# Kernel tuning notes

Hardware: AMD Instinct MI355X
Metric: run time of the kernel (lower is better)

Reference implementation:

```python
import jax, jax.numpy as jnp
import numpy as np

B_SZ = 4; SEQ = 2048; SPLIT = 1024
D_MODEL = 512; N_LAYERS = 2; EXPAND = 2
D_INNER = EXPAND * D_MODEL          # 1024
HEADDIM = 64; NHEADS = D_INNER // HEADDIM   # 16
DSTATE = 64; CONV = 4; CHUNK = 256
D_INPROJ = 2 * D_INNER + 2 * DSTATE + NHEADS   # z, xBC, dt
CONVDIM = D_INNER + 2 * DSTATE
NHID = 1024; NOUT = 10; CA_HEADS = 4; CA_HD = D_MODEL // CA_HEADS


def _ln(x, w, b, eps=1e-5):
    m = jnp.mean(x, -1, keepdims=True)
    v = jnp.mean(jnp.square(x - m), -1, keepdims=True)
    return (x - m) * jax.lax.rsqrt(v + eps) * w + b


def _segsum(x):
    # x: (..., T) -> (..., T, T) lower-triangular cumulative segment sums
    T = x.shape[-1]
    xc = jnp.cumsum(x, -1)
    ss = xc[..., :, None] - xc[..., None, :]
    mask = jnp.tril(jnp.ones((T, T), bool))
    return jnp.where(mask, ss, -jnp.inf)


def _ssd(x, A, B, C):
    # chunked SSD (Mamba2). x:(b,l,h,p) dt-prescaled; A:(b,l,h)=dt*A; B,C:(b,l,n)
    b, l, h, p = x.shape
    n = B.shape[-1]
    c = l // CHUNK
    x = x.reshape(b, c, CHUNK, h, p)
    A = jnp.transpose(A.reshape(b, c, CHUNK, h), (0, 1, 3, 2))   # (b,c,h,L)
    B = B.reshape(b, c, CHUNK, n)
    C = C.reshape(b, c, CHUNK, n)
    A_cum = jnp.cumsum(A, -1)
    Lmat = jnp.exp(_segsum(A))                                    # (b,c,h,L,L)
    Y_diag = jnp.einsum('bcln,bcsn,bchls,bcshp->bclhp', C, B, Lmat, x)
    decay_states = jnp.exp(A_cum[..., -1:] - A_cum)               # (b,c,h,L)
    states = jnp.einsum('bcln,bchl,bclhp->bchpn', B, decay_states, x)
    chunk_decay = jnp.exp(A_cum[..., -1])                         # (b,c,h)
    def step(hprev, inp):
        dec, s = inp
        return hprev * dec[..., None, None] + s, hprev
    init = jnp.zeros((b, h, p, n), x.dtype)
    _, prev = jax.lax.scan(step, init,
                           (jnp.moveaxis(chunk_decay, 1, 0), jnp.moveaxis(states, 1, 0)))
    prev = jnp.moveaxis(prev, 0, 1)                               # (b,c,h,p,n) state at chunk start
    Y_off = jnp.einsum('bcln,bchpn,bchl->bclhp', C, prev, jnp.exp(A_cum))
    return (Y_diag + Y_off).reshape(b, l, h, p)


def _mamba2_dir(u, Win, cw, cb, dtb, Alog, Dp, gw, Wout):
    b, l, _ = u.shape
    zxbcdt = u @ Win
    z, xBC, dt_raw = jnp.split(zxbcdt, [D_INNER, D_INNER + CONVDIM], -1)
    # causal depthwise conv, kernel CONV
    xp = jnp.pad(xBC, ((0, 0), (CONV - 1, 0), (0, 0)))
    xc = cb + sum(xp[:, k:k + l, :] * cw[:, k] for k in range(CONV))
    xc = jax.nn.silu(xc)
    x, Bm, Cm = jnp.split(xc, [D_INNER, D_INNER + DSTATE], -1)
    dt = jax.nn.softplus(dt_raw + dtb)                            # (b,l,h)
    A = -jnp.exp(Alog)                                            # (h,)
    xh = x.reshape(b, l, NHEADS, HEADDIM)
    y = _ssd(xh * dt[..., None], dt * A, Bm, Cm) + Dp[None, None, :, None] * xh
    y = y.reshape(b, l, D_INNER) * jax.nn.silu(z)                 # gated
    y = y * jax.lax.rsqrt(jnp.mean(jnp.square(y), -1, keepdims=True) + 1e-5) * gw
    return y @ Wout


def _cross_attn(q_in, c_in, nqw, nqb, nkvw, nkvb, qw, qb, kw, kb, vw, vb, ow, ob):
    res = q_in
    q = _ln(q_in, nqw, nqb)
    c = _ln(c_in, nkvw, nkvb)
    Bq, Nq, D = q.shape
    Nc = c.shape[1]
    Q = (q @ qw + qb).reshape(Bq, Nq, CA_HEADS, CA_HD)
    K = (c @ kw + kb).reshape(Bq, Nc, CA_HEADS, CA_HD)
    V = (c @ vw + vb).reshape(Bq, Nc, CA_HEADS, CA_HD)
    attn = jax.nn.softmax(jnp.einsum('bqhd,bkhd->bhqk', Q, K) / np.float32(np.sqrt(CA_HD)), -1)
    out = jnp.einsum('bhqk,bkhd->bqhd', attn, V).reshape(Bq, Nq, D)
    return res + out @ ow + ob


def _forward(x_enc, split_pos, in_proj_w, conv_w, conv_b, dt_bias, A_log, D_param,
             gnorm_w, out_proj_w, norm_w, norm_b, normf_w, normf_b,
             ca_nq_w, ca_nq_b, ca_nkv_w, ca_nkv_b, ca_qw, ca_qb, ca_kw, ca_kb,
             ca_vw, ca_vb, ca_ow, ca_ob, qp_w, qp_b, cp_w, cp_b,
             dec1_w, dec1_b, dec2_w, dec2_b):
    h = x_enc
    res = None
    for i in range(N_LAYERS):
        res = h if res is None else h + res
        hn = _ln(res, norm_w[i], norm_b[i])
        fwd = _mamba2_dir(hn, in_proj_w[i, 0], conv_w[i, 0], conv_b[i, 0], dt_bias[i, 0],
                          A_log[i, 0], D_param[i, 0], gnorm_w[i, 0], out_proj_w[i, 0])
        bwd = _mamba2_dir(jnp.flip(hn, 1), in_proj_w[i, 1], conv_w[i, 1], conv_b[i, 1],
                          dt_bias[i, 1], A_log[i, 1], D_param[i, 1], gnorm_w[i, 1], out_proj_w[i, 1])
        h = fwd + jnp.flip(bwd, 1)
    res = h + res
    h = _ln(res, normf_w, normf_b)
    context = h[:, :split_pos]
    query = h[:, split_pos:]
    q = query @ qp_w + qp_b
    c = context @ cp_w + cp_b
    out = _cross_attn(q, c, ca_nq_w, ca_nq_b, ca_nkv_w, ca_nkv_b,
                      ca_qw, ca_qb, ca_kw, ca_kb, ca_vw, ca_vb, ca_ow, ca_ob)
    out = jax.nn.gelu(out @ dec1_w + dec1_b, approximate=False) @ dec2_w + dec2_b
    return out


def setup_inputs() -> dict:
    key = jax.random.key(0)
    ks = iter(jax.random.split(key, 64))
    def nrm(shape, scale=0.02):
        return jax.random.normal(next(ks), shape, jnp.float32) * scale
    L2 = (N_LAYERS, 2)
    inp = {}
    inp['x_enc'] = jax.random.normal(next(ks), (B_SZ, SEQ, D_MODEL), jnp.float32)
    inp['split_pos'] = SPLIT
    inp['in_proj_w'] = nrm(L2 + (D_MODEL, D_INPROJ))
    inp['conv_w'] = nrm(L2 + (CONVDIM, CONV), 0.1)
    inp['conv_b'] = jnp.zeros(L2 + (CONVDIM,), jnp.float32)
    inp['dt_bias'] = nrm(L2 + (NHEADS,), 0.5)
    inp['A_log'] = jnp.log(jnp.broadcast_to(jnp.arange(1, NHEADS + 1, dtype=jnp.float32), L2 + (NHEADS,)))
    inp['D_param'] = jnp.ones(L2 + (NHEADS,), jnp.float32)
    inp['gnorm_w'] = jnp.ones(L2 + (D_INNER,), jnp.float32)
    inp['out_proj_w'] = nrm(L2 + (D_INNER, D_MODEL))
    inp['norm_w'] = jnp.ones((N_LAYERS, D_MODEL), jnp.float32)
    inp['norm_b'] = jnp.zeros((N_LAYERS, D_MODEL), jnp.float32)
    inp['normf_w'] = jnp.ones((D_MODEL,), jnp.float32)
    inp['normf_b'] = jnp.zeros((D_MODEL,), jnp.float32)
    inp['ca_nq_w'] = jnp.ones((D_MODEL,), jnp.float32); inp['ca_nq_b'] = jnp.zeros((D_MODEL,), jnp.float32)
    inp['ca_nkv_w'] = jnp.ones((D_MODEL,), jnp.float32); inp['ca_nkv_b'] = jnp.zeros((D_MODEL,), jnp.float32)
    for nm in ['ca_qw', 'ca_kw', 'ca_vw', 'ca_ow']:
        inp[nm] = nrm((D_MODEL, D_MODEL))
    for nm in ['ca_qb', 'ca_kb', 'ca_vb', 'ca_ob']:
        inp[nm] = jnp.zeros((D_MODEL,), jnp.float32)
    inp['qp_w'] = nrm((D_MODEL, D_MODEL)); inp['qp_b'] = jnp.zeros((D_MODEL,), jnp.float32)
    inp['cp_w'] = nrm((D_MODEL, D_MODEL)); inp['cp_b'] = jnp.zeros((D_MODEL,), jnp.float32)
    inp['dec1_w'] = nrm((D_MODEL, NHID)); inp['dec1_b'] = jnp.zeros((NHID,), jnp.float32)
    inp['dec2_w'] = nrm((NHID, NOUT)); inp['dec2_b'] = jnp.zeros((NOUT,), jnp.float32)
    return inp


def reference(x_enc, split_pos, in_proj_w, conv_w, conv_b, dt_bias, A_log, D_param,
              gnorm_w, out_proj_w, norm_w, norm_b, normf_w, normf_b,
              ca_nq_w, ca_nq_b, ca_nkv_w, ca_nkv_b, ca_qw, ca_qb, ca_kw, ca_kb,
              ca_vw, ca_vb, ca_ow, ca_ob, qp_w, qp_b, cp_w, cp_b,
              dec1_w, dec1_b, dec2_w, dec2_b):
    return _forward(x_enc, split_pos, in_proj_w, conv_w, conv_b, dt_bias, A_log, D_param,
                    gnorm_w, out_proj_w, norm_w, norm_b, normf_w, normf_b,
                    ca_nq_w, ca_nq_b, ca_nkv_w, ca_nkv_b, ca_qw, ca_qb, ca_kw, ca_kb,
                    ca_vw, ca_vb, ca_ow, ca_ob, qp_w, qp_b, cp_w, cp_b,
                    dec1_w, dec1_b, dec2_w, dec2_b)
```

## Files before the change

kernel.cpp:

```cpp
#include <hip/hip_runtime.h>
#include <hip/hip_bf16.h>

#define BS 4
#define SEQL 2048
#define DM 512
#define DIN 1024
#define NH 16
#define HD 64
#define DST 64
#define NC 8
#define CKS 256
#define DIP 2192
#define CVD 1152
#define NROWS (BS*SEQL)
#define NTOK (BS*SEQL*DM)

typedef unsigned short u16;
typedef __bf16 bf16x8 __attribute__((ext_vector_type(8)));
typedef float f32x4 __attribute__((ext_vector_type(4)));

__device__ __forceinline__ u16 cvt_bf16(float f){
  unsigned int x = __float_as_uint(f);
  unsigned int r = x + 0x7fffu + ((x>>16)&1u);
  return (u16)(r>>16);
}
__device__ __forceinline__ float bf2f(u16 u){
  return __uint_as_float(((unsigned int)u)<<16);
}

__global__ void k_add_flip(float* __restrict__ dst, const float* __restrict__ src, int flip){
  int i = blockIdx.x*256 + threadIdx.x;
  if(i >= NTOK) return;
  int d = i & (DM-1);
  int l = (i >> 9) & (SEQL-1);
  int b = i >> 20;
  int sl = flip ? (SEQL-1-l) : l;
  dst[i] += src[(b*SEQL + sl)*DM + d];
}

__global__ void k_flip(float* __restrict__ dst, const float* __restrict__ src){
  int i = blockIdx.x*256 + threadIdx.x;
  if(i >= NTOK) return;
  int d = i & (DM-1);
  int l = (i >> 9) & (SEQL-1);
  int b = i >> 20;
  dst[i] = src[(b*SEQL + (SEQL-1-l))*DM + d];
}

__global__ void k_cvt(const float* __restrict__ src, u16* __restrict__ dst, int n4){
  int i = blockIdx.x*256 + threadIdx.x;
  if(i >= n4) return;
  float4 f = reinterpret_cast<const float4*>(src)[i];
  ushort4 o; o.x=cvt_bf16(f.x); o.y=cvt_bf16(f.y); o.z=cvt_bf16(f.z); o.w=cvt_bf16(f.w);
  reinterpret_cast<ushort4*>(dst)[i] = o;
}

__global__ void k_ln(const float* __restrict__ X, const float* __restrict__ w,
                     const float* __restrict__ bb, float* __restrict__ O){
  int row = blockIdx.x, tid = threadIdx.x;
  const float* x = X + (size_t)row*DM;
  float* o = O + (size_t)row*DM;
  float s=0.f, s2=0.f;
  for(int j=tid;j<DM;j+=256){ float v=x[j]; s+=v; s2+=v*v; }
  __shared__ float r1[256], r2[256];
  r1[tid]=s; r2[tid]=s2; __syncthreads();
  for(int off=128;off>0;off>>=1){
    if(tid<off){ r1[tid]+=r1[tid+off]; r2[tid]+=r2[tid+off]; }
    __syncthreads();
  }
  float m = r1[0]*(1.f/DM);
  float var = r2[0]*(1.f/DM) - m*m;
  float inv = rsqrtf(var + 1e-5f);
  for(int j=tid;j<DM;j+=256) o[j] = (x[j]-m)*inv*w[j] + bb[j];
}

__global__ void k_rms(float* __restrict__ Y, const float* __restrict__ gw){
  int row = blockIdx.x, tid = threadIdx.x;
  float* y = Y + (size_t)row*DIN;
  float ss=0.f;
  for(int j=tid;j<DIN;j+=256){ float v=y[j]; ss+=v*v; }
  __shared__ float red[256];
  red[tid]=ss; __syncthreads();
  for(int off=128;off>0;off>>=1){
    if(tid<off) red[tid]+=red[tid+off];
    __syncthreads();
  }
  float inv = rsqrtf(red[0]*(1.f/DIN) + 1e-5f);
  for(int j=tid;j<DIN;j+=256) y[j] = y[j]*inv*gw[j];
}

__global__ void k_dec2(const float* __restrict__ D1, const float* __restrict__ w,
                       const float* __restrict__ bb, float* __restrict__ out){
  int row = blockIdx.x, tid = threadIdx.x;
  int lane = tid & 63, wave = tid >> 6;
  const float* x = D1 + (size_t)row*1024;
  float acc[10];
  #pragma unroll
  for(int o=0;o<10;o++) acc[o]=0.f;
  for(int j=tid;j<1024;j+=256){
    float v = x[j];
    const float* wr = w + (size_t)j*10;
    #pragma unroll
    for(int o=0;o<10;o++) acc[o] += v*wr[o];
  }
  __shared__ float red[4][10];
  #pragma unroll
  for(int o=0;o<10;o++){
    float v = acc[o];
    #pragma unroll
    for(int s=32;s>0;s>>=1) v += __shfl_down(v, s, 64);
    if(lane==0) red[wave][o] = v;
  }
  __syncthreads();
  if(tid < 10)
    out[(size_t)row*10 + tid] = red[0][tid]+red[1][tid]+red[2][tid]+red[3][tid] + bb[tid];
}

__global__ void k_wt2(const float* __restrict__ src, u16* __restrict__ dst,
                      int K, int N, int lds){
  __shared__ float t[32][33];
  int n0 = blockIdx.x*32, k0 = blockIdx.y*32;
  int tx = threadIdx.x, ty = threadIdx.y;
  #pragma unroll
  for(int i=0;i<32;i+=8){
    int k = k0+ty+i, n = n0+tx;
    t[ty+i][tx] = (n<N) ? src[(size_t)k*lds+n] : 0.f;
  }
  __syncthreads();
  #pragma unroll
  for(int i=0;i<32;i+=8){
    int n = n0+ty+i, k = k0+tx;
    if(n<N) dst[(size_t)n*K+k] = cvt_bf16(t[tx][ty+i]);
  }
}

__global__ void k_vtb(const float* __restrict__ VV, u16* __restrict__ VT){
  __shared__ float t[32][33];
  int z = blockIdx.z, b = z>>2, h = z&3;
  const float* src = VV + (size_t)b*524288 + h*128;
  u16* dst = VT + (size_t)z*131072;
  int n0 = blockIdx.x*32, k0 = blockIdx.y*32;
  int tx = threadIdx.x, ty = threadIdx.y;
  #pragma unroll
  for(int i=0;i<32;i+=8){
    int k = k0+ty+i, n = n0+tx;
    t[ty+i][tx] = src[(size_t)k*512+n];
  }
  __syncthreads();
  #pragma unroll
  for(int i=0;i<32;i+=8){
    int n = n0+ty+i, k = k0+tx;
    dst[(size_t)n*1024+k] = cvt_bf16(t[tx][ty+i]);
  }
}

__global__ void k_xdtt(const float* __restrict__ XC, const float* __restrict__ DT,
                       u16* __restrict__ XdT){
  __shared__ float t[32][33];
  int z = blockIdx.z;
  int h = z & 15, bc = z >> 4;
  int b = bc >> 3, c = bc & 7;
  int p0 = blockIdx.x*32, s0 = blockIdx.y*32;
  int tx = threadIdx.x, ty = threadIdx.y;
  int gbase = b*SEQL + c*CKS;
  #pragma unroll
  for(int i=0;i<32;i+=8){
    int s = s0+ty+i, p = p0+tx;
    int g = gbase + s;
    t[ty+i][tx] = XC[(size_t)g*CVD + h*HD + p] * DT[(size_t)g*NH + h];
  }
  __syncthreads();
  u16* dst = XdT + (size_t)z*16384;
  #pragma unroll
  for(int i=0;i<32;i+=8){
    int p = p0+ty+i, s = s0+tx;
    dst[(size_t)p*256 + s] = cvt_bf16(t[tx][ty+i]);
  }
}

__global__ __launch_bounds__(256) void k_mg(
    const u16* __restrict__ A, const u16* __restrict__ BT,
    float* __restrict__ C, int M, int N, int K, int lda, int ldb, int ldc)
{
  __shared__ uint4 As4[128*5];
  __shared__ uint4 Bs4[128*5];
  const int tid = threadIdx.x;
  const int row0 = blockIdx.y*128, col0 = blockIdx.x*128;
  const int lane = tid & 63, wave = tid >> 6;
  const int wm = wave >> 1, wn = wave & 1;
  const int lr = lane & 15, ksg = (lane >> 4);
  f32x4 acc[4][4];
  #pragma unroll
  for(int i=0;i<4;i++)
    #pragma unroll
    for(int j=0;j<4;j++) acc[i][j] = (f32x4){0.f,0.f,0.f,0.f};
  for(int k0=0;k0<K;k0+=32){
    #pragma unroll
    for(int i=0;i<2;i++){
      int t2 = tid + i*256;
      int rr = t2 >> 2, sg = (t2 & 3);
      uint4 av = *reinterpret_cast<const uint4*>(A + (size_t)(row0+rr)*lda + k0 + sg*8);
      uint4 bv = {0u,0u,0u,0u};
      if(col0+rr < N) bv = *reinterpret_cast<const uint4*>(BT + (size_t)(col0+rr)*ldb + k0 + sg*8);
      As4[rr*5 + sg] = av;
      Bs4[rr*5 + sg] = bv;
    }
    __syncthreads();
    bf16x8 afr[4], bfr[4];
    #pragma unroll
    for(int i=0;i<4;i++) afr[i] = *reinterpret_cast<const bf16x8*>(&As4[(wm*64+i*16+lr)*5 + ksg]);
    #pragma unroll
    for(int j=0;j<4;j++) bfr[j] = *reinterpret_cast<const bf16x8*>(&Bs4[(wn*64+j*16+lr)*5 + ksg]);
    #pragma unroll
    for(int i=0;i<4;i++)
      #pragma unroll
      for(int j=0;j<4;j++)
        acc[i][j] = __builtin_amdgcn_mfma_f32_16x16x32_bf16(afr[i], bfr[j], acc[i][j], 0, 0, 0);
    __syncthreads();
  }
  const int hi = lane >> 4, lo = lane & 15;
  #pragma unroll
  for(int i=0;i<4;i++)
    #pragma unroll
    for(int j=0;j<4;j++)
      #pragma unroll
      for(int r=0;r<4;r++){
        int row = row0 + wm*64 + i*16 + 4*hi + r;
        int col = col0 + wn*64 + j*16 + lo;
        if(col < N) C[(size_t)row*ldc + col] = acc[i][j][r];
      }
}

__global__ __launch_bounds__(256) void k_mgb(
    const u16* __restrict__ A0, const u16* __restrict__ BT0,
    float* __restrict__ C0, int M, int N, int K, int lda, int ldb, int ldc,
    long sAz, long sBz, long sCo, long sCi, int shC)
{
  const int z = blockIdx.z;
  const u16* A  = A0  + (size_t)z*sAz;
  const u16* BT = BT0 + (size_t)z*sBz;
  float* C = C0 + (size_t)(z>>shC)*sCo + (size_t)(z & ((1<<shC)-1))*sCi;
  __shared__ uint4 As4[128*5];
  __shared__ uint4 Bs4[128*5];
  const int tid = threadIdx.x;
  const int row0 = blockIdx.y*128, col0 = blockIdx.x*128;
  const int lane = tid & 63, wave = tid >> 6;
  const int wm = wave >> 1, wn = wave & 1;
  const int lr = lane & 15, ksg = (lane >> 4);
  f32x4 acc[4][4];
  #pragma unroll
  for(int i=0;i<4;i++)
    #pragma unroll
    for(int j=0;j<4;j++) acc[i][j] = (f32x4){0.f,0.f,0.f,0.f};
  for(int k0=0;k0<K;k0+=32){
    #pragma unroll
    for(int i=0;i<2;i++){
      int t2 = tid + i*256;
      int rr = t2 >> 2, sg = (t2 & 3);
      uint4 av = *reinterpret_cast<const uint4*>(A + (size_t)(row0+rr)*lda + k0 + sg*8);
      uint4 bv = {0u,0u,0u,0u};
      if(col0+rr < N) bv = *reinterpret_cast<const uint4*>(BT + (size_t)(col0+rr)*ldb + k0 + sg*8);
      As4[rr*5 + sg] = av;
      Bs4[rr*5 + sg] = bv;
    }
    __syncthreads();
    bf16x8 afr[4], bfr[4];
    #pragma unroll
    for(int i=0;i<4;i++) afr[i] = *reinterpret_cast<const bf16x8*>(&As4[(wm*64+i*16+lr)*5 + ksg]);
    #pragma unroll
    for(int j=0;j<4;j++) bfr[j] = *reinterpret_cast<const bf16x8*>(&Bs4[(wn*64+j*16+lr)*5 + ksg]);
    #pragma unroll
    for(int i=0;i<4;i++)
      #pragma unroll
      for(int j=0;j<4;j++)
        acc[i][j] = __builtin_amdgcn_mfma_f32_16x16x32_bf16(afr[i], bfr[j], acc[i][j], 0, 0, 0);
    __syncthreads();
  }
  const int hi = lane >> 4, lo = lane & 15;
  #pragma unroll
  for(int i=0;i<4;i++)
    #pragma unroll
    for(int j=0;j<4;j++)
      #pragma unroll
      for(int r=0;r<4;r++){
        int row = row0 + wm*64 + i*16 + 4*hi + r;
        int col = col0 + wn*64 + j*16 + lo;
        if(col < N) C[(size_t)row*ldc + col] = acc[i][j][r];
      }
}

__global__ __launch_bounds__(256) void k_mgg(
    const float* __restrict__ Sf, const float* __restrict__ ACUM,
    const u16* __restrict__ XdT, float* __restrict__ Y)
{
  const int z = blockIdx.z;
  const int h = z & 15, bc = z >> 4;
  const int b = bc >> 3, c = bc & 7;
  const float* Az = Sf + (size_t)bc*65536;
  const float* Acp = ACUM + (size_t)z*256;
  const u16* BT = XdT + (size_t)z*16384;
  float* Cp = Y + (size_t)b*2097152 + (size_t)c*262144 + h*64;
  __shared__ uint4 As4[128*5];
  __shared__ uint4 Bs4[128*5];
  __shared__ float AcS[256];
  const int tid = threadIdx.x;
  AcS[tid] = Acp[tid];
  __syncthreads();
  const int row0 = blockIdx.y*128;
  const int lane = tid & 63, wave = tid >> 6;
  const int wm = wave >> 1, wn = wave & 1;
  const int lr = lane & 15, ksg = (lane >> 4);
  f32x4 acc[4][4];
  #pragma unroll
  for(int i=0;i<4;i++)
    #pragma unroll
    for(int j=0;j<4;j++) acc[i][j] = (f32x4){0.f,0.f,0.f,0.f};
  for(int k0=0;k0<256;k0+=32){
    #pragma unroll
    for(int i=0;i<2;i++){
      int t2 = tid + i*256;
      int rr = t2 >> 2, sg = (t2 & 3);
      int l = row0 + rr;
      int sbase = k0 + sg*8;
      float4 v0 = *reinterpret_cast<const float4*>(Az + (size_t)l*256 + sbase);
      float4 v1 = *reinterpret_cast<const float4*>(Az + (size_t)l*256 + sbase + 4);
      float acl = AcS[l];
      float vv[8] = {v0.x,v0.y,v0.z,v0.w,v1.x,v1.y,v1.z,v1.w};
      u16 gbuf[8];
      #pragma unroll
      for(int e=0;e<8;e++){
        int s = sbase + e;
        float g = 0.f;
        if(s <= l) g = __expf(acl - AcS[s]) * vv[e];
        gbuf[e] = cvt_bf16(g);
      }
      As4[rr*5 + sg] = *reinterpret_cast<uint4*>(gbuf);
      uint4 bv = {0u,0u,0u,0u};
      if(rr < 64) bv = *reinterpret_cast<const uint4*>(BT + (size_t)rr*256 + sbase);
      Bs4[rr*5 + sg] = bv;
    }
    __syncthreads();
    bf16x8 afr[4], bfr[4];
    #pragma unroll
    for(int i=0;i<4;i++) afr[i] = *reinterpret_cast<const bf16x8*>(&As4[(wm*64+i*16+lr)*5 + ksg]);
    #pragma unroll
    for(int j=0;j<4;j++) bfr[j] = *reinterpret_cast<const bf16x8*>(&Bs4[(wn*64+j*16+lr)*5 + ksg]);
    #pragma unroll
    for(int i=0;i<4;i++)
      #pragma unroll
      for(int j=0;j<4;j++)
        acc[i][j] = __builtin_amdgcn_mfma_f32_16x16x32_bf16(afr[i], bfr[j], acc[i][j], 0, 0, 0);
    __syncthreads();
  }
  const int hi = lane >> 4, lo = lane & 15;
  #pragma unroll
  for(int i=0;i<4;i++)
    #pragma unroll
    for(int j=0;j<4;j++)
      #pragma unroll
      for(int r=0;r<4;r++){
        int row = row0 + wm*64 + i*16 + 4*hi + r;
        int col = wn*64 + j*16 + lo;
        if(col < 64) Cp[(size_t)row*1024 + col] = acc[i][j][r];
      }
}

__global__ __launch_bounds__(256) void k_mgab(
    const u16* __restrict__ A0, const u16* __restrict__ BT0,
    float* __restrict__ C0, u16* __restrict__ Cb0,
    int M, int N, int K, int lda, int ldb, int ldc,
    long sAo, long sAi, long sBo, long sBi, long sCo, long sCi, float scale)
{
  const int z = blockIdx.z;
  const u16* A  = A0  + (size_t)(z>>2)*sAo + (size_t)(z&3)*sAi;
  const u16* BT = BT0 + (size_t)(z>>2)*sBo + (size_t)(z&3)*sBi;
  const size_t offC = (size_t)(z>>2)*sCo + (size_t)(z&3)*sCi;
  __shared__ uint4 As4[128*5];
  __shared__ uint4 Bs4[128*5];
  const int tid = threadIdx.x;
  const int row0 = blockIdx.y*128, col0 = blockIdx.x*128;
  const int lane = tid & 63, wave = tid >> 6;
  const int wm = wave >> 1, wn = wave & 1;
  const int lr = lane & 15, ksg = (lane >> 4);
  f32x4 acc[4][4];
  #pragma unroll
  for(int i=0;i<4;i++)
    #pragma unroll
    for(int j=0;j<4;j++) acc[i][j] = (f32x4){0.f,0.f,0.f,0.f};
  for(int k0=0;k0<K;k0+=32){
    #pragma unroll
    for(int i=0;i<2;i++){
      int t2 = tid + i*256;
      int rr = t2 >> 2, sg = (t2 & 3);
      uint4 av = *reinterpret_cast<const uint4*>(A + (size_t)(row0+rr)*lda + k0 + sg*8);
      uint4 bv = {0u,0u,0u,0u};
      if(col0+rr < N) bv = *reinterpret_cast<const uint4*>(BT + (size_t)(col0+rr)*ldb + k0 + sg*8);
      As4[rr*5 + sg] = av;
      Bs4[rr*5 + sg] = bv;
    }
    __syncthreads();
    bf16x8 afr[4], bfr[4];
    #pragma unroll
    for(int i=0;i<4;i++) afr[i] = *reinterpret_cast<const bf16x8*>(&As4[(wm*64+i*16+lr)*5 + ksg]);
    #pragma unroll
    for(int j=0;j<4;j++) bfr[j] = *reinterpret_cast<const bf16x8*>(&Bs4[(wn*64+j*16+lr)*5 + ksg]);
    #pragma unroll
    for(int i=0;i<4;i++)
      #pragma unroll
      for(int j=0;j<4;j++)
        acc[i][j] = __builtin_amdgcn_mfma_f32_16x16x32_bf16(afr[i], bfr[j], acc[i][j], 0, 0, 0);
    __syncthreads();
  }
  const int hi = lane >> 4, lo = lane & 15;
  #pragma unroll
  for(int i=0;i<4;i++)
    #pragma unroll
    for(int j=0;j<4;j++)
      #pragma unroll
      for(int r=0;r<4;r++){
        int row = row0 + wm*64 + i*16 + 4*hi + r;
        int col = col0 + wn*64 + j*16 + lo;
        if(col < N){
          float v = acc[i][j][r] * scale;
          size_t ci = offC + (size_t)row*ldc + col;
          if(C0) C0[ci] = v;
          else   Cb0[ci] = cvt_bf16(v);
        }
      }
}

__global__ __launch_bounds__(256) void k_mgy(
    const u16* __restrict__ Cb0, const u16* __restrict__ PV0,
    const float* __restrict__ ACUM, const float* __restrict__ XCp,
    const float* __restrict__ ZBp, const float* __restrict__ Dp,
    float* __restrict__ Y)
{
  const int z = blockIdx.z;
  const int b = z>>3, c = z&7;
  const u16* A  = Cb0 + (size_t)z*16384;
  const u16* BT = PV0 + (size_t)z*65536;
  const int N = 1024;
  __shared__ uint4 As4[128*5];
  __shared__ uint4 Bs4[128*5];
  const int tid = threadIdx.x;
  const int row0 = blockIdx.y*128, col0 = blockIdx.x*128;
  const int lane = tid & 63, wave = tid >> 6;
  const int wm = wave >> 1, wn = wave & 1;
  const int lr = lane & 15, ksg = (lane >> 4);
  f32x4 acc[4][4];
  #pragma unroll
  for(int i=0;i<4;i++)
    #pragma unroll
    for(int j=0;j<4;j++) acc[i][j] = (f32x4){0.f,0.f,0.f,0.f};
  for(int k0=0;k0<64;k0+=32){
    #pragma unroll
    for(int i=0;i<2;i++){
      int t2 = tid + i*256;
      int rr = t2 >> 2, sg = (t2 & 3);
      uint4 av = *reinterpret_cast<const uint4*>(A + (size_t)(row0+rr)*64 + k0 + sg*8);
      uint4 bv = {0u,0u,0u,0u};
      if(col0+rr < N) bv = *reinterpret_cast<const uint4*>(BT + (size_t)(col0+rr)*64 + k0 + sg*8);
      As4[rr*5 + sg] = av;
      Bs4[rr*5 + sg] = bv;
    }
    __syncthreads();
    bf16x8 afr[4], bfr[4];
    #pragma unroll
    for(int i=0;i<4;i++) afr[i] = *reinterpret_cast<const bf16x8*>(&As4[(wm*64+i*16+lr)*5 + ksg]);
    #pragma unroll
    for(int j=0;j<4;j++) bfr[j] = *reinterpret_cast<const bf16x8*>(&Bs4[(wn*64+j*16+lr)*5 + ksg]);
    #pragma unroll
    for(int i=0;i<4;i++)
      #pragma unroll
      for(int j=0;j<4;j++)
        acc[i][j] = __builtin_amdgcn_mfma_f32_16x16x32_bf16(afr[i], bfr[j], acc[i][j], 0, 0, 0);
    __syncthreads();
  }
  const int hi = lane >> 4, lo = lane & 15;
  #pragma unroll
  for(int i=0;i<4;i++)
    #pragma unroll
    for(int j=0;j<4;j++)
      #pragma unroll
      for(int r=0;r<4;r++){
        int row = row0 + wm*64 + i*16 + 4*hi + r;
        int col = col0 + wn*64 + j*16 + lo;
        int h = col >> 6;
        int g = b*SEQL + c*CKS + row;
        float ac = ACUM[((size_t)z*NH + h)*CKS + row];
        float xh = XCp[(size_t)g*CVD + col];
        float zg = ZBp[(size_t)g*DIP + col];
        size_t ci = (size_t)g*DIN + col;
        float v = Y[ci] + expf(ac)*acc[i][j][r] + Dp[h]*xh;
        float sig = 1.f/(1.f+expf(-zg));
        Y[ci] = v * (zg*sig);
      }
}

__global__ __launch_bounds__(256) void k_mge(
    const u16* __restrict__ A, const u16* __restrict__ BT,
    const float* __restrict__ bias, const float* __restrict__ res,
    float* __restrict__ C, u16* __restrict__ Cbf,
    int M, int N, int K, int lda, int ldb, int ldc, float scale, int act)
{
  __shared__ uint4 As4[128*5];
  __shared__ uint4 Bs4[128*5];
  const int tid = threadIdx.x;
  const int row0 = blockIdx.y*128, col0 = blockIdx.x*128;
  const int lane = tid & 63, wave = tid >> 6;
  const int wm = wave >> 1, wn = wave & 1;
  const int lr = lane & 15, ksg = (lane >> 4);
  f32x4 acc[4][4];
  #pragma unroll
  for(int i=0;i<4;i++)
    #pragma unroll
    for(int j=0;j<4;j++) acc[i][j] = (f32x4){0.f,0.f,0.f,0.f};
  for(int k0=0;k0<K;k0+=32){
    #pragma unroll
    for(int i=0;i<2;i++){
      int t2 = tid + i*256;
      int rr = t2 >> 2, sg = (t2 & 3);
      uint4 av = *reinterpret_cast<const uint4*>(A + (size_t)(row0+rr)*lda + k0 + sg*8);
      uint4 bv = {0u,0u,0u,0u};
      if(col0+rr < N) bv = *reinterpret_cast<const uint4*>(BT + (size_t)(col0+rr)*ldb + k0 + sg*8);
      As4[rr*5 + sg] = av;
      Bs4[rr*5 + sg] = bv;
    }
    __syncthreads();
    bf16x8 afr[4], bfr[4];
    #pragma unroll
    for(int i=0;i<4;i++) afr[i] = *reinterpret_cast<const bf16x8*>(&As4[(wm*64+i*16+lr)*5 + ksg]);
    #pragma unroll
    for(int j=0;j<4;j++) bfr[j] = *reinterpret_cast<const bf16x8*>(&Bs4[(wn*64+j*16+lr)*5 + ksg]);
    #pragma unroll
    for(int i=0;i<4;i++)
      #pragma unroll
      for(int j=0;j<4;j++)
        acc[i][j] = __builtin_amdgcn_mfma_f32_16x16x32_bf16(afr[i], bfr[j], acc[i][j], 0, 0, 0);
    __syncthreads();
  }
  const int hi = lane >> 4, lo = lane & 15;
  #pragma unroll
  for(int i=0;i<4;i++)
    #pragma unroll
    for(int j=0;j<4;j++)
      #pragma unroll
      for(int r=0;r<4;r++){
        int row = row0 + wm*64 + i*16 + 4*hi + r;
        int col = col0 + wn*64 + j*16 + lo;
        if(col < N){
          float v = acc[i][j][r];
          if(bias) v += bias[col];
          v *= scale;
          if(act==1) v = 0.5f*v*(1.f+erff(v*0.70710678118654752f));
          size_t ci = (size_t)row*ldc + col;
          if(res) v += res[ci];
          if(C) C[ci] = v;
          else  Cbf[ci] = cvt_bf16(v);
        }
      }
}

__global__ void k_sm(u16* __restrict__ S){
  size_t row = blockIdx.x;
  u16* p = S + row*1024;
  int tid = threadIdx.x;
  ushort4 u = reinterpret_cast<ushort4*>(p)[tid];
  float v0=bf2f(u.x), v1=bf2f(u.y), v2=bf2f(u.z), v3=bf2f(u.w);
  float m = fmaxf(fmaxf(v0,v1),fmaxf(v2,v3));
  __shared__ float red[256];
  red[tid]=m; __syncthreads();
  for(int o=128;o>0;o>>=1){ if(tid<o) red[tid]=fmaxf(red[tid],red[tid+o]); __syncthreads(); }
  m = red[0]; __syncthreads();
  v0=__expf(v0-m); v1=__expf(v1-m); v2=__expf(v2-m); v3=__expf(v3-m);
  float s = v0+v1+v2+v3;
  red[tid]=s; __syncthreads();
  for(int o=128;o>0;o>>=1){ if(tid<o) red[tid]+=red[tid+o]; __syncthreads(); }
  float inv = 1.f/red[0];
  ushort4 o4; o4.x=cvt_bf16(v0*inv); o4.y=cvt_bf16(v1*inv); o4.z=cvt_bf16(v2*inv); o4.w=cvt_bf16(v3*inv);
  reinterpret_cast<ushort4*>(p)[tid] = o4;
}

__global__ void k_conv4(const float* __restrict__ ZB, const float* __restrict__ cw,
                        const float* __restrict__ cb, float* __restrict__ XC){
  int i = blockIdx.x*256 + threadIdx.x;
  if(i >= BS*512*CVD) return;
  int cch = i % CVD;
  int lq = (i / CVD) & 511;
  int b = i / (CVD*512);
  int l0 = lq*4;
  float w[7];
  #pragma unroll
  for(int t=0;t<7;t++){
    int sl = l0 - 3 + t;
    w[t] = (sl >= 0) ? ZB[(size_t)(b*SEQL+sl)*DIP + DIN + cch] : 0.f;
  }
  float c0 = cw[cch*4+0], c1 = cw[cch*4+1], c2 = cw[cch*4+2], c3 = cw[cch*4+3];
  float bb2 = cb[cch];
  #pragma unroll
  for(int j=0;j<4;j++){
    float v = bb2 + w[j]*c0 + w[j+1]*c1 + w[j+2]*c2 + w[j+3]*c3;
    float sig = 1.f/(1.f+expf(-v));
    XC[(size_t)(b*SEQL + l0 + j)*CVD + cch] = v*sig;
  }
}

__global__ void k_dt(const float* __restrict__ ZB, const float* __restrict__ dtb,
                     const float* __restrict__ Alog, float* __restrict__ DT,
                     float* __restrict__ DA){
  int i = blockIdx.x*256 + threadIdx.x;
  if(i >= BS*SEQL*NH) return;
  int h = i & (NH-1);
  int row = i >> 4;
  float raw = ZB[(size_t)row*DIP + (DIN+CVD) + h] + dtb[h];
  float dt = fmaxf(raw,0.f) + log1pf(expf(-fabsf(raw)));
  DT[i] = dt;
  DA[i] = dt * (-expf(Alog[h]));
}

__global__ void k_acum(const float* __restrict__ DA, float* __restrict__ ACUM,
                       float* __restrict__ CDEC){
  int blk = blockIdx.x;
  int h = blk & 15, c = (blk>>4)&7, b = blk>>7;
  int l = threadIdx.x;
  __shared__ float s[256];
  int gl = c*CKS + l;
  s[l] = DA[(size_t)(b*SEQL + gl)*NH + h];
  __syncthreads();
  for(int off=1; off<256; off<<=1){
    float v = (l>=off) ? s[l-off] : 0.f;
    __syncthreads();
    s[l] += v;
    __syncthreads();
  }
  ACUM[(size_t)blk*CKS + l] = s[l];
  if(l==255) CDEC[blk] = expf(s[255]);
}

__global__ void k_bc(const float* __restrict__ XC, u16* __restrict__ Bbf,
                     u16* __restrict__ Cbf){
  int i = blockIdx.x*256 + threadIdx.x;
  if(i >= NROWS*DST) return;
  int g = i >> 6, n = i & 63;
  Bbf[i] = cvt_bf16(XC[(size_t)g*CVD + DIN + n]);
  Cbf[i] = cvt_bf16(XC[(size_t)g*CVD + DIN + DST + n]);
}

__global__ void k_states(const float* __restrict__ XC, const float* __restrict__ DT,
                         const float* __restrict__ ACUM, float* __restrict__ ST){
  int blk = blockIdx.x;
  int h = blk & 15, c = (blk>>4)&7, b = blk>>7;
  int tid = threadIdx.x;
  int n = tid & 63, pq = tid >> 6;
  __shared__ float Ac[256];
  __shared__ float Bt[32][64];
  __shared__ float Xt[32][64];
  Ac[tid] = ACUM[(size_t)blk*CKS + tid];
  float acc[16];
  #pragma unroll
  for(int k=0;k<16;k++) acc[k]=0.f;
  const float* xcb = XC + (size_t)b*SEQL*CVD;
  for(int st=0; st<8; ++st){
    __syncthreads();
    #pragma unroll
    for(int e=0;e<8;e++){
      int idx = tid + e*256;
      int sl = idx>>6, nn = idx&63;
      int gs = c*CKS + st*32 + sl;
      Bt[sl][nn] = xcb[(size_t)gs*CVD + DIN + nn];
      float dec = expf(Ac[255] - Ac[st*32+sl]);
      Xt[sl][nn] = xcb[(size_t)gs*CVD + h*HD + nn] * DT[(size_t)(b*SEQL+gs)*NH + h] * dec;
    }
    __syncthreads();
    #pragma unroll
    for(int l=0;l<32;l++){
      float bv = Bt[l][n];
      #pragma unroll
      for(int k=0;k<16;k++) acc[k] += bv * Xt[l][pq + 4*k];
    }
  }
  #pragma unroll
  for(int k=0;k<16;k++){
    int p = pq + 4*k;
    ST[(size_t)blk*4096 + p*64 + n] = acc[k];
  }
}

__global__ void k_scan(const float* __restrict__ ST, const float* __restrict__ CDEC,
                       float* __restrict__ PREV){
  int i = blockIdx.x*256 + threadIdx.x;
  if(i >= BS*NH*4096) return;
  int pn = i & 4095;
  int h = (i>>12) & 15;
  int b = i >> 16;
  float run = 0.f;
  for(int c=0;c<8;c++){
    size_t idx = (size_t)((b*8+c)*16+h)*4096 + pn;
    PREV[idx] = run;
    run = run*CDEC[(b*8+c)*16+h] + ST[idx];
  }
}

__global__ void k_extract(const float* __restrict__ HF, float* __restrict__ QIN,
                          float* __restrict__ CIN){
  int i = blockIdx.x*256 + threadIdx.x;
  if(i >= BS*1024*DM) return;
  int d = i & (DM-1);
  int q = (i>>9) & 1023;
  int b = i >> 19;
  QIN[i] = HF[(size_t)(b*SEQL + 1024 + q)*DM + d];
  CIN[i] = HF[(size_t)(b*SEQL + q)*DM + d];
}

extern "C" void kernel_launch(void* const* d_in, const int* in_sizes, int n_in,
                              void* d_out, int out_size, void* d_ws, size_t ws_size,
                              hipStream_t stream) {
  (void)in_sizes; (void)n_in; (void)out_size; (void)ws_size;
  const float* x_enc     = (const float*)d_in[0];
  const float* in_proj_w = (const float*)d_in[2];
  const float* conv_w    = (const float*)d_in[3];
  const float* conv_b    = (const float*)d_in[4];
  const float* dt_bias   = (const float*)d_in[5];
  const float* A_log     = (const float*)d_in[6];
  const float* D_param   = (const float*)d_in[7];
  const float* gnorm_w   = (const float*)d_in[8];
  const float* out_proj_w= (const float*)d_in[9];
  const float* norm_w    = (const float*)d_in[10];
  const float* norm_b    = (const float*)d_in[11];
  const float* normf_w   = (const float*)d_in[12];
  const float* normf_b   = (const float*)d_in[13];
  const float* ca_nq_w   = (const float*)d_in[14];
  const float* ca_nq_b   = (const float*)d_in[15];
  const float* ca_nkv_w  = (const float*)d_in[16];
  const float* ca_nkv_b  = (const float*)d_in[17];
  const float* ca_qw     = (const float*)d_in[18];
  const float* ca_kw     = (const float*)d_in[19];
  const float* ca_vw     = (const float*)d_in[20];
  const float* ca_ow     = (const float*)d_in[21];
  const float* ca_qb     = (const float*)d_in[22];
  const float* ca_kb     = (const float*)d_in[23];
  const float* ca_vb     = (const float*)d_in[24];
  const float* ca_ob     = (const float*)d_in[25];
  const float* qp_w      = (const float*)d_in[26];
  const float* qp_b      = (const float*)d_in[27];
  const float* cp_w      = (const float*)d_in[28];
  const float* cp_b      = (const float*)d_in[29];
  const float* dec1_w    = (const float*)d_in[30];
  const float* dec1_b    = (const float*)d_in[31];
  const float* dec2_w    = (const float*)d_in[32];
  const float* dec2_b    = (const float*)d_in[33];

  float* W = (float*)d_ws;
  size_t off = 0;
  auto alloc = [&](size_t n){ float* pp = W + off; off += n; return pp; };
  float* RES  = alloc((size_t)NTOK);
  float* H    = alloc((size_t)NTOK);
  float* HN   = alloc((size_t)NTOK);
  float* HNF  = alloc((size_t)NTOK);
  float* ZB   = alloc((size_t)NROWS*DIP);
  float* XC   = alloc((size_t)NROWS*CVD);
  float* DT   = alloc((size_t)NROWS*NH);
  float* DA   = alloc((size_t)NROWS*NH);
  float* ACUM = alloc((size_t)BS*NC*NH*CKS);
  float* CDEC = alloc((size_t)BS*NC*NH);
  float* Y    = alloc((size_t)NROWS*DIN);
  float* ST   = alloc((size_t)BS*NC*NH*4096);
  float* PREV = alloc((size_t)BS*NC*NH*4096);
  float* YD   = alloc((size_t)NTOK);
  float* HF   = alloc((size_t)NTOK);

  u16* Ubf    = (u16*)HF;
  u16* WinTc  = (u16*)(HF + 2097152);
  u16* WoutTc = (u16*)(HF + 2097152 + 561152);
  u16* Ybf    = (u16*)HNF;
  u16*   Bbf    = (u16*)HNF;
  u16*   Cbf    = Bbf + 524288;
  float* Sf     = HNF + 524288;
  u16*   PREVbf = (u16*)Sf;
  u16*   XdTg   = (u16*)YD;

  const int TPB = 256;
  const int gTok = (NTOK+TPB-1)/TPB;
  dim3 tb(32,8);

  hipMemcpyAsync(RES, x_enc, (size_t)NTOK*4, hipMemcpyDeviceToDevice, stream);

  for(int layer=0; layer<2; ++layer){
    if(layer>0) k_add_flip<<<gTok,TPB,0,stream>>>(RES, H, 0);
    k_ln<<<NROWS,TPB,0,stream>>>(RES, norm_w + layer*DM, norm_b + layer*DM, HN);
    hipMemsetAsync(H, 0, (size_t)NTOK*4, stream);
    for(int dir=0; dir<2; ++dir){
      int idx = layer*2 + dir;
      const float* cw   = conv_w   + (size_t)idx*CVD*4;
      const float* cb   = conv_b   + (size_t)idx*CVD;
      const float* dtb  = dt_bias  + (size_t)idx*NH;
      const float* Alog = A_log    + (size_t)idx*NH;
      const float* Dp   = D_param  + (size_t)idx*NH;
      const float* gw   = gnorm_w  + (size_t)idx*DIN;

      if(dir==0){
        k_cvt<<<(NTOK/4+TPB-1)/TPB,TPB,0,stream>>>(HN, Ubf, NTOK/4);
      }else{
        k_flip<<<gTok,TPB,0,stream>>>(HNF, HN);
        k_cvt<<<(NTOK/4+TPB-1)/TPB,TPB,0,stream>>>(HNF, Ubf, NTOK/4);
      }
      k_wt2<<<dim3(69,16),tb,0,stream>>>(in_proj_w + (size_t)idx*DM*DIP, WinTc, 512, 2192, 2192);
      k_mg<<<dim3(18,64),256,0,stream>>>(Ubf, WinTc, ZB, 8192, 2192, 512, 512, 512, 2192);

      k_conv4<<<(BS*512*CVD+TPB-1)/TPB,TPB,0,stream>>>(ZB, cw, cb, XC);
      k_dt<<<(BS*SEQL*NH+TPB-1)/TPB,TPB,0,stream>>>(ZB, dtb, Alog, DT, DA);
      k_acum<<<BS*NC*NH,256,0,stream>>>(DA, ACUM, CDEC);

      k_bc<<<(NROWS*DST+TPB-1)/TPB,TPB,0,stream>>>(XC, Bbf, Cbf);
      k_mgb<<<dim3(2,2,32),256,0,stream>>>(Cbf, Bbf, Sf,
            256, 256, 64, 64, 64, 256, 16384, 16384, 65536, 0, 0);
      k_xdtt<<<dim3(2,8,512),tb,0,stream>>>(XC, DT, XdTg);
      k_mgg<<<dim3(1,2,512),256,0,stream>>>(Sf, ACUM, XdTg, Y);

      k_states<<<BS*NC*NH,256,0,stream>>>(XC, DT, ACUM, ST);
      k_scan<<<(BS*NH*4096+TPB-1)/TPB,TPB,0,stream>>>(ST, CDEC, PREV);
      k_cvt<<<(2097152/4+TPB-1)/TPB,TPB,0,stream>>>(PREV, PREVbf, 2097152/4);
      k_mgy<<<dim3(8,2,32),256,0,stream>>>(Cbf, PREVbf, ACUM, XC, ZB, Dp, Y);

      k_rms<<<NROWS,256,0,stream>>>(Y, gw);

      k_cvt<<<(2097152+TPB-1)/TPB,TPB,0,stream>>>(Y, Ybf, 2097152);
      k_wt2<<<dim3(16,32),tb,0,stream>>>(out_proj_w + (size_t)idx*DIN*DM, WoutTc, 1024, 512, 512);
      k_mg<<<dim3(4,64),256,0,stream>>>(Ybf, WoutTc, YD, 8192, 512, 1024, 1024, 1024, 512);

      k_add_flip<<<gTok,TPB,0,stream>>>(H, YD, dir);
    }
  }
  k_add_flip<<<gTok,TPB,0,stream>>>(RES, H, 0);
  k_ln<<<NROWS,TPB,0,stream>>>(RES, normf_w, normf_b, HF);

  float* P0   = ZB;
  float* QIN  = P0 + 0;
  float* CIN  = P0 + 2097152;
  float* QPb  = P0 + 4194304;
  float* CPb  = P0 + 6291456;
  float* QN   = P0 + 8388608;
  float* CN   = P0 + 10485760;
  float* AO   = P0 + 12582912;
  float* O1   = P0 + 14680064;
  float* D1   = P0 + 16777216;
  float* VV   = D1;
  u16* U0     = (u16*)(P0 + 20971520);
  u16* Qbf    = U0 + 0;
  u16* Cbf2   = U0 + 2097152;
  u16* QNbf   = U0 + 4194304;
  u16* CNbf   = U0 + 6291456;
  u16* QQbf   = U0 + 8388608;
  u16* KKbf   = U0 + 10485760;
  u16* VTbf   = U0 + 12582912;
  u16* AObf   = U0 + 14680064;
  u16* O1bf   = U0 + 16777216;
  u16* qpT    = U0 + 18874368;
  u16* cpT    = qpT + 262144;
  u16* qwT    = qpT + 524288;
  u16* kwT    = qpT + 786432;
  u16* vwT    = qpT + 1048576;
  u16* owT    = qpT + 1310720;
  u16* dec1T  = qpT + 1572864;
  u16* Pbf    = qpT + 2097152;

  const int M2 = BS*1024;
  k_extract<<<(BS*1024*DM+TPB-1)/TPB,TPB,0,stream>>>(HF, QIN, CIN);
  k_cvt<<<(2097152/4+TPB-1)/TPB,TPB,0,stream>>>(QIN, Qbf, 2097152/4);
  k_cvt<<<(2097152/4+TPB-1)/TPB,TPB,0,stream>>>(CIN, Cbf2, 2097152/4);
  k_wt2<<<dim3(16,16),tb,0,stream>>>(qp_w, qpT, 512, 512, 512);
  k_wt2<<<dim3(16,16),tb,0,stream>>>(cp_w, cpT, 512, 512, 512);
  k_wt2<<<dim3(16,16),tb,0,stream>>>(ca_qw, qwT, 512, 512, 512);
  k_wt2<<<dim3(16,16),tb,0,stream>>>(ca_kw, kwT, 512, 512, 512);
  k_wt2<<<dim3(16,16),tb,0,stream>>>(ca_vw, vwT, 512, 512, 512);
  k_wt2<<<dim3(16,16),tb,0,stream>>>(ca_ow, owT, 512, 512, 512);
  k_wt2<<<dim3(32,16),tb,0,stream>>>(dec1_w, dec1T, 512, 1024, 1024);

  k_mge<<<dim3(4,32),256,0,stream>>>(Qbf, qpT, qp_b, nullptr, QPb, nullptr,
                                     M2, 512, 512, 512, 512, 512, 1.f, 0);
  k_mge<<<dim3(4,32),256,0,stream>>>(Cbf2, cpT, cp_b, nullptr, CPb, nullptr,
                                     M2, 512, 512, 512, 512, 512, 1.f, 0);
  k_ln<<<M2,TPB,0,stream>>>(QPb, ca_nq_w, ca_nq_b, QN);
  k_ln<<<M2,TPB,0,stream>>>(CPb, ca_nkv_w, ca_nkv_b, CN);
  k_cvt<<<(2097152/4+TPB-1)/TPB,TPB,0,stream>>>(QN, QNbf, 2097152/4);
  k_cvt<<<(2097152/4+TPB-1)/TPB,TPB,0,stream>>>(CN, CNbf, 2097152/4);
  k_mge<<<dim3(4,32),256,0,stream>>>(QNbf, qwT, ca_qb, nullptr, nullptr, QQbf,
                                     M2, 512, 512, 512, 512, 512, 1.f, 0);
  k_mge<<<dim3(4,32),256,0,stream>>>(CNbf, kwT, ca_kb, nullptr, nullptr, KKbf,
                                     M2, 512, 512, 512, 512, 512, 1.f, 0);
  k_mge<<<dim3(4,32),256,0,stream>>>(CNbf, vwT, ca_vb, nullptr, VV, nullptr,
                                     M2, 512, 512, 512, 512, 512, 1.f, 0);
  k_vtb<<<dim3(4,32,16),tb,0,stream>>>(VV, VTbf);
  const float scl = 0.088388347648318447f;
  k_mgab<<<dim3(8,8,16),256,0,stream>>>(QQbf, KKbf, nullptr, Pbf,
        1024, 1024, 128, 512, 512, 1024,
        524288, 128, 524288, 128, 4194304, 1048576, scl);
  k_sm<<<16384,256,0,stream>>>(Pbf);
  k_mgab<<<dim3(1,8,16),256,0,stream>>>(Pbf, VTbf, AO, nullptr,
        1024, 128, 1024, 1024, 1024, 512,
        4194304, 1048576, 524288, 131072, 524288, 128, 1.f);
  k_cvt<<<(2097152/4+TPB-1)/TPB,TPB,0,stream>>>(AO, AObf, 2097152/4);
  k_mge<<<dim3(4,32),256,0,stream>>>(AObf, owT, ca_ob, QPb, O1, nullptr,
                                     M2, 512, 512, 512, 512, 512, 1.f, 0);
  k_cvt<<<(2097152/4+TPB-1)/TPB,TPB,0,stream>>>(O1, O1bf, 2097152/4);
  k_mge<<<dim3(8,32),256,0,stream>>>(O1bf, dec1T, dec1_b, nullptr, D1, nullptr,
                                     M2, 1024, 512, 512, 512, 1024, 1.f, 1);
  k_dec2<<<M2,256,0,stream>>>(D1, dec2_w, dec2_b, (float*)d_out);
}
```

Measured before the change: 1.545 ms.

## Compute chunk states with bf16 MFMA GEMM reusing transposed dt-scaled X

```diff
diff --git a/kernel.cpp b/kernel.cpp
--- a/kernel.cpp
+++ b/kernel.cpp
@@ -175,6 +175,26 @@
   for(int i=0;i<32;i+=8){
     int p = p0+ty+i, s = s0+tx;
     dst[(size_t)p*256 + s] = cvt_bf16(t[tx][ty+i]);
+  }
+}
+
+__global__ void k_btc(const u16* __restrict__ Bbf, u16* __restrict__ BTc){
+  __shared__ u16 t[32][33];
+  int bc = blockIdx.z;
+  const u16* src = Bbf + (size_t)bc*16384;
+  u16* dst = BTc + (size_t)bc*16384;
+  int n0 = blockIdx.x*32, l0 = blockIdx.y*32;
+  int tx = threadIdx.x, ty = threadIdx.y;
+  #pragma unroll
+  for(int i=0;i<32;i+=8){
+    int l = l0+ty+i, n = n0+tx;
+    t[ty+i][tx] = src[(size_t)l*64+n];
+  }
+  __syncthreads();
+  #pragma unroll
+  for(int i=0;i<32;i+=8){
+    int n = n0+ty+i, l = l0+tx;
+    dst[(size_t)n*256+l] = t[tx][ty+i];
   }
 }
 
@@ -365,6 +385,78 @@
       }
 }
 
+__global__ __launch_bounds__(256) void k_mgs(
+    const u16* __restrict__ XdT, const u16* __restrict__ BTc,
+    const float* __restrict__ ACUM, float* __restrict__ ST)
+{
+  const int z = blockIdx.z;
+  const int bc = z >> 4;
+  const u16* Ap = XdT + (size_t)z*16384;
+  const u16* BT = BTc + (size_t)bc*16384;
+  float* Cp = ST + (size_t)z*4096;
+  __shared__ uint4 As4[128*5];
+  __shared__ uint4 Bs4[128*5];
+  __shared__ float decS[256];
+  const int tid = threadIdx.x;
+  {
+    const float* Acp = ACUM + (size_t)z*256;
+    decS[tid] = __expf(Acp[255] - Acp[tid]);
+  }
+  __syncthreads();
+  const int lane = tid & 63, wave = tid >> 6;
+  const int wm = wave >> 1, wn = wave & 1;
+  const int lr = lane & 15, ksg = (lane >> 4);
+  f32x4 acc[4][4];
+  #pragma unroll
+  for(int i=0;i<4;i++)
+    #pragma unroll
+    for(int j=0;j<4;j++) acc[i][j] = (f32x4){0.f,0.f,0.f,0.f};
+  for(int k0=0;k0<256;k0+=32){
+    #pragma unroll
+    for(int i=0;i<2;i++){
+      int t2 = tid + i*256;
+      int rr = t2 >> 2, sg = (t2 & 3);
+      int sbase = k0 + sg*8;
+      uint4 av = {0u,0u,0u,0u};
+      if(rr < 64){
+        uint4 raw = *reinterpret_cast<const uint4*>(Ap + (size_t)rr*256 + sbase);
+        const u16* rp = reinterpret_cast<const u16*>(&raw);
+        u16 buf[8];
+        #pragma unroll
+        for(int e=0;e<8;e++) buf[e] = cvt_bf16(bf2f(rp[e]) * decS[sbase+e]);
+        av = *reinterpret_cast<uint4*>(buf);
+      }
+      As4[rr*5 + sg] = av;
+      uint4 bv = {0u,0u,0u,0u};
+      if(rr < 64) bv = *reinterpret_cast<const uint4*>(BT + (size_t)rr*256 + sbase);
+      Bs4[rr*5 + sg] = bv;
+    }
+    __syncthreads();
+    bf16x8 afr[4], bfr[4];
+    #pragma unroll
+    for(int i=0;i<4;i++) afr[i] = *reinterpret_cast<const bf16x8*>(&As4[(wm*64+i*16+lr)*5 + ksg]);
+    #pragma unroll
+    for(int j=0;j<4;j++) bfr[j] = *reinterpret_cast<const bf16x8*>(&Bs4[(wn*64+j*16+lr)*5 + ksg]);
+    #pragma unroll
+    for(int i=0;i<4;i++)
+      #pragma unroll
+      for(int j=0;j<4;j++)
+        acc[i][j] = __builtin_amdgcn_mfma_f32_16x16x32_bf16(afr[i], bfr[j], acc[i][j], 0, 0, 0);
+    __syncthreads();
+  }
+  const int hi = lane >> 4, lo = lane & 15;
+  #pragma unroll
+  for(int i=0;i<4;i++)
+    #pragma unroll
+    for(int j=0;j<4;j++)
+      #pragma unroll
+      for(int r=0;r<4;r++){
+        int row = wm*64 + i*16 + 4*hi + r;
+        int col = wn*64 + j*16 + lo;
+        if(row < 64 && col < 64) Cp[(size_t)row*64 + col] = acc[i][j][r];
+      }
+}
+
 __global__ __launch_bounds__(256) void k_mgab(
     const u16* __restrict__ A0, const u16* __restrict__ BT0,
     float* __restrict__ C0, u16* __restrict__ Cb0,
@@ -644,46 +736,6 @@
   int g = i >> 6, n = i & 63;
   Bbf[i] = cvt_bf16(XC[(size_t)g*CVD + DIN + n]);
   Cbf[i] = cvt_bf16(XC[(size_t)g*CVD + DIN + DST + n]);
-}
-
-__global__ void k_states(const float* __restrict__ XC, const float* __restrict__ DT,
-                         const float* __restrict__ ACUM, float* __restrict__ ST){
-  int blk = blockIdx.x;
-  int h = blk & 15, c = (blk>>4)&7, b = blk>>7;
-  int tid = threadIdx.x;
-  int n = tid & 63, pq = tid >> 6;
-  __shared__ float Ac[256];
-  __shared__ float Bt[32][64];
-  __shared__ float Xt[32][64];
-  Ac[tid] = ACUM[(size_t)blk*CKS + tid];
-  float acc[16];
-  #pragma unroll
-  for(int k=0;k<16;k++) acc[k]=0.f;
-  const float* xcb = XC + (size_t)b*SEQL*CVD;
-  for(int st=0; st<8; ++st){
-    __syncthreads();
-    #pragma unroll
-    for(int e=0;e<8;e++){
-      int idx = tid + e*256;
-      int sl = idx>>6, nn = idx&63;
-      int gs = c*CKS + st*32 + sl;
-      Bt[sl][nn] = xcb[(size_t)gs*CVD + DIN + nn];
-      float dec = expf(Ac[255] - Ac[st*32+sl]);
-      Xt[sl][nn] = xcb[(size_t)gs*CVD + h*HD + nn] * DT[(size_t)(b*SEQL+gs)*NH + h] * dec;
-    }
-    __syncthreads();
-    #pragma unroll
-    for(int l=0;l<32;l++){
-      float bv = Bt[l][n];
-      #pragma unroll
-      for(int k=0;k<16;k++) acc[k] += bv * Xt[l][pq + 4*k];
-    }
-  }
-  #pragma unroll
-  for(int k=0;k<16;k++){
-    int p = pq + 4*k;
-    ST[(size_t)blk*4096 + p*64 + n] = acc[k];
-  }
 }
 
 __global__ void k_scan(const float* __restrict__ ST, const float* __restrict__ CDEC,
@@ -777,6 +829,7 @@
   u16*   Cbf    = Bbf + 524288;
   float* Sf     = HNF + 524288;
   u16*   PREVbf = (u16*)Sf;
+  u16*   BTc    = (u16*)(HNF + 2621440);
   u16*   XdTg   = (u16*)YD;
 
   const int TPB = 256;
@@ -817,7 +870,8 @@
       k_xdtt<<<dim3(2,8,512),tb,0,stream>>>(XC, DT, XdTg);
       k_mgg<<<dim3(1,2,512),256,0,stream>>>(Sf, ACUM, XdTg, Y);
 
-      k_states<<<BS*NC*NH,256,0,stream>>>(XC, DT, ACUM, ST);
+      k_btc<<<dim3(2,8,32),tb,0,stream>>>(Bbf, BTc);
+      k_mgs<<<dim3(1,1,512),256,0,stream>>>(XdTg, BTc, ACUM, ST);
       k_scan<<<(BS*NH*4096+TPB-1)/TPB,TPB,0,stream>>>(ST, CDEC, PREV);
       k_cvt<<<(2097152/4+TPB-1)/TPB,TPB,0,stream>>>(PREV, PREVbf, 2097152/4);
       k_mgy<<<dim3(8,2,32),256,0,stream>>>(Cbf, PREVbf, ACUM, XC, ZB, Dp, Y);
```

New measurement: 1.445 ms. -6.5%, faster.
